# Kernel tuning notes

Hardware: AMD Instinct MI355X
Metric: run time of the kernel (lower is better)

The kernel has to match this reference:

```python
import jax, jax.numpy as jnp
import numpy as np

N_NODES = 100000
N_EDGES = 1600000
IN_CH = 128
HID = 128
OUT_CH = 64
N_GRAPHS = 512


def gcn_conv(x, edge_index, W, b):
    # GCNConv (PyG defaults): add self-loops, symmetric normalization
    # out = D^{-1/2} (A + I) D^{-1/2} X W + b
    n = x.shape[0]
    loop = jnp.arange(n, dtype=edge_index.dtype)
    src = jnp.concatenate([edge_index[0], loop])
    dst = jnp.concatenate([edge_index[1], loop])
    deg = jax.ops.segment_sum(jnp.ones_like(dst, x.dtype), dst, num_segments=n)
    dinv = jnp.where(deg > 0, jax.lax.rsqrt(deg), jnp.zeros_like(deg))
    norm = dinv[src] * dinv[dst]            # [E+N]
    h = x @ W                                # [N, out] transform first (dense GEMM)
    msg = h[src] * norm[:, None]             # gather + scale  [E+N, out]
    return jax.ops.segment_sum(msg, dst, num_segments=n) + b


def global_mean_pool(x, batch, num_graphs):
    sums = jax.ops.segment_sum(x, batch, num_segments=num_graphs)
    cnts = jax.ops.segment_sum(jnp.ones_like(batch, x.dtype), batch, num_segments=num_graphs)
    return sums / jnp.maximum(cnts, 1.0)[:, None]


def setup_inputs() -> dict:
    key = jax.random.key(0)
    ks = jax.random.split(key, 12)
    x = jax.random.normal(ks[0], (N_NODES, IN_CH), dtype=jnp.float32)
    edge_index = jax.random.randint(ks[1], (2, N_EDGES), 0, N_NODES, dtype=jnp.int64)
    batch = jnp.sort(jax.random.randint(ks[2], (N_NODES,), 0, N_GRAPHS, dtype=jnp.int64))
    def glorot(k, fi, fo):
        s = float(np.sqrt(6.0 / (fi + fo)))
        return jax.random.uniform(k, (fi, fo), jnp.float32, -s, s)
    W1 = glorot(ks[3], IN_CH, HID); b1 = jnp.zeros((HID,), jnp.float32)
    W2 = glorot(ks[4], HID, HID);   b2 = jnp.zeros((HID,), jnp.float32)
    W3 = glorot(ks[5], HID, HID);   b3 = jnp.zeros((HID,), jnp.float32)
    W4 = glorot(ks[6], HID, OUT_CH); b4 = jnp.zeros((OUT_CH,), jnp.float32)
    return {"x": x, "edge_index": edge_index, "batch": batch,
            "W1": W1, "b1": b1, "W2": W2, "b2": b2,
            "W3": W3, "b3": b3, "W4": W4, "b4": b4}


def reference(x, edge_index, batch, W1, b1, W2, b2, W3, b3, W4, b4):
    h = jax.nn.relu(gcn_conv(x, edge_index, W1, b1))
    h = jax.nn.relu(gcn_conv(h, edge_index, W2, b2))
    g = global_mean_pool(h, batch, N_GRAPHS)           # [G, HID]
    # MLP head; Dropout(0.2) is identity in eval mode
    g = jax.nn.relu(g @ W3 + b3)
    return g @ W4 + b4                                  # [G, OUT_CH]
```

## Files before the change

kernel.cpp:

```cpp
#include <hip/hip_runtime.h>

#define NN 100000
#define EE 1600000
#define CH 128
#define NG 512
#define OC 64

#define CSH 10
#define NCB 98
#define PBLK 256
#define PCHUNK 6250
#define SCAP 128
#define NCG 8
#define CPG 32
#define DSL 100352

#define O_DINV   0
#define O_ROWS   100032
#define O_CNT    200064
#define O_PART   225152
#define O_OFFS   225280
#define O_START  225408
#define O_CSR    225984
#define O_HS     2726016
#define O_STG    9126080
#define O_A1     14800448
#define O_DEG8   21200448
#define O_DEG    22003264
#define O_WT1    22103616
#define O_WT2    22120000

typedef __attribute__((ext_vector_type(8))) short short8v;
typedef __attribute__((ext_vector_type(4))) float float4v;

static __device__ __forceinline__ unsigned short f2bf(float x) {
  unsigned u = __float_as_uint(x);
  return (unsigned short)((u + 0x7FFFu + ((u >> 16) & 1u)) >> 16);
}
static __device__ __forceinline__ float bf2f(unsigned short h) {
  return __uint_as_float((unsigned)h << 16);
}
static __device__ __forceinline__ unsigned pack2(float a, float b) {
  return (unsigned)f2bf(a) | ((unsigned)f2bf(b) << 16);
}
static __device__ __forceinline__ float bflo(unsigned v) {
  return __uint_as_float(v << 16);
}
static __device__ __forceinline__ float bfhi(unsigned v) {
  return __uint_as_float(v & 0xFFFF0000u);
}

__global__ __launch_bounds__(1024) void k_part(const int* __restrict__ src,
                                               const int* __restrict__ dst,
                                               int* __restrict__ cnt,
                                               unsigned* __restrict__ stg) {
  __shared__ int hist[NCB];
  __shared__ int lcur[NCB];
  __shared__ unsigned lout[PCHUNK];
  int t = threadIdx.x;
  int e0 = blockIdx.x * PCHUNK;
  if (t < NCB) { hist[t] = 0; lcur[t] = 0; }
  __syncthreads();
  for (int e = e0 + t; e < e0 + PCHUNK; e += 1024)
    atomicAdd(&hist[dst[e] >> CSH], 1);
  __syncthreads();
  if (t == 0) {
    int s = 0;
    for (int i = 0; i < NCB; ++i) { int v = hist[i]; hist[i] = s; s += v; }
  }
  __syncthreads();
  for (int e = e0 + t; e < e0 + PCHUNK; e += 1024) {
    int d = dst[e];
    int b = d >> CSH;
    int p = hist[b] + atomicAdd(&lcur[b], 1);
    lout[p] = (unsigned)src[e] | ((unsigned)(d & 1023) << 17);
  }
  __syncthreads();
  int w = t >> 6, lane = t & 63;
  unsigned* mystg = stg + (size_t)blockIdx.x * NCB * SCAP;
  for (int b = w; b < NCB; b += 16) {
    int beg = hist[b];
    int end = (b == NCB - 1) ? PCHUNK : hist[b + 1];
    int n = min(end - beg, SCAP);
    for (int i = lane; i < n; i += 64) mystg[b * SCAP + i] = lout[beg + i];
    if (lane == 0) cnt[blockIdx.x * NCB + b] = n;
  }
}

__global__ __launch_bounds__(1024) void k_count2(const unsigned* __restrict__ stg,
                                                 const int* __restrict__ cnt,
                                                 int* __restrict__ deg8) {
  __shared__ int ldeg[1024];
  int b = blockIdx.x, g = blockIdx.y;
  int t = threadIdx.x;
  int w = t >> 6, lane = t & 63;
  ldeg[t] = 0;
  __syncthreads();
  for (int blk = g * CPG + w; blk < (g + 1) * CPG; blk += 16) {
    int c = cnt[blk * NCB + b];
    const unsigned* p = stg + ((size_t)blk * NCB + b) * SCAP;
    for (int e = lane; e < c; e += 64) atomicAdd(&ldeg[p[e] >> 17], 1);
  }
  __syncthreads();
  deg8[g * DSL + (b << CSH) + t] = ldeg[t];
}

__global__ __launch_bounds__(1024) void k_scan1(const int* __restrict__ deg8,
                                                int* __restrict__ deg,
                                                int* __restrict__ rows,
                                                int* __restrict__ part,
                                                float* __restrict__ dinv) {
  __shared__ int s[1024];
  int b = blockIdx.x, t = threadIdx.x;
  int gid = (b << CSH) + t;
  int v = 0;
#pragma unroll
  for (int g = 0; g < NCG; ++g) v += deg8[g * DSL + gid];
  if (gid < NN) {
    dinv[gid] = rsqrtf((float)(v + 1));
    deg[gid] = v;
  }
  int pdeg = (v + 7) & ~7;
  s[t] = pdeg;
  __syncthreads();
  for (int off = 1; off < 1024; off <<= 1) {
    int u = (t >= off) ? s[t - off] : 0;
    __syncthreads();
    if (t >= off) s[t] += u;
    __syncthreads();
  }
  if (gid < NN) rows[gid] = s[t] - pdeg;
  if (t == 1023) part[b] = s[t];
}

__global__ void k_scan_part(const int* __restrict__ part, int* __restrict__ offs) {
  __shared__ int s[128];
  int t = threadIdx.x;
  int v = (t < NCB) ? part[t] : 0;
  s[t] = v;
  __syncthreads();
  for (int off = 1; off < 128; off <<= 1) {
    int u = (t >= off) ? s[t - off] : 0;
    __syncthreads();
    if (t >= off) s[t] += u;
    __syncthreads();
  }
  if (t < NCB) offs[t] = s[t] - v;
}

__global__ void k_scan_add(int* __restrict__ rows, const int* __restrict__ offs,
                           const int* __restrict__ part, const int* __restrict__ deg,
                           const int* __restrict__ batch, int* __restrict__ start,
                           int* __restrict__ csr,
                           const float* __restrict__ W1, const float* __restrict__ W2,
                           unsigned short* __restrict__ wt1,
                           unsigned short* __restrict__ wt2) {
  int i = blockIdx.x * 256 + threadIdx.x;
  if (i >= NN) return;
  if (i < 32768) {
    const float* W = (i < 16384) ? W1 : W2;
    unsigned short* wt = (i < 16384) ? wt1 : wt2;
    int ii = i & 16383;
    int k = ii >> 7, n = ii & 127;
    float w = W[ii];
    unsigned short h = f2bf(w);
    unsigned short l = f2bf(w - bf2f(h));
    wt[n * 128 + k] = h;
    wt[16384 + n * 128 + k] = l;
  }
  int r = rows[i] + offs[i >> 10];
  rows[i] = r;
  if (i == 0) rows[NN] = offs[NCB - 1] + part[NCB - 1];
  int d = deg[i];
  int pd = (d + 7) & ~7;
  for (int k = r + d; k < r + pd; ++k) csr[k] = NN;
  int b = batch[i];
  int prev = (i == 0) ? -1 : batch[i - 1];
  for (int g = prev + 1; g <= b; ++g) start[g] = i;
  if (i == NN - 1)
    for (int g = b + 1; g <= NG; ++g) start[g] = NN;
}

__global__ __launch_bounds__(1024) void k_place2(const unsigned* __restrict__ stg,
                                                 const int* __restrict__ cnt,
                                                 const int* __restrict__ rows,
                                                 const int* __restrict__ deg8,
                                                 int* __restrict__ csr) {
  __shared__ int lrow[1024];
  __shared__ int lcur[1024];
  int b = blockIdx.x, g = blockIdx.y;
  int t = threadIdx.x;
  int w = t >> 6, lane = t & 63;
  int gid = (b << CSH) + t;
  int base = (gid < NN) ? rows[gid] : 0;
  for (int gp = 0; gp < g; ++gp) base += deg8[gp * DSL + gid];
  lrow[t] = base;
  lcur[t] = 0;
  __syncthreads();
  for (int blk = g * CPG + w; blk < (g + 1) * CPG; blk += 16) {
    int c = cnt[blk * NCB + b];
    const unsigned* p = stg + ((size_t)blk * NCB + b) * SCAP;
    for (int e = lane; e < c; e += 64) {
      unsigned x = p[e];
      int ld = x >> 17;
      int q = atomicAdd(&lcur[ld], 1);
      csr[lrow[ld] + q] = (int)(x & 0x1FFFFu);
    }
  }
}

__global__ __launch_bounds__(256) void k_gemm_mfma(
    const float* __restrict__ X, const unsigned short* __restrict__ wth,
    const unsigned short* __restrict__ wtl, const float* __restrict__ dinv,
    unsigned short* __restrict__ Hs) {
  __shared__ __align__(16) unsigned short sWh[64 * 136];
  __shared__ __align__(16) unsigned short sWl[64 * 136];
  __shared__ __align__(16) unsigned short sXh[128 * 40];
  __shared__ __align__(16) unsigned short sXl[128 * 40];

  const int t = threadIdx.x;
  const int w = t >> 6, lane = t & 63;
  const int quad = lane >> 4, lr = lane & 15;
  const int row0 = blockIdx.x * 128;
  const int col0 = blockIdx.y * 64;

  if (blockIdx.x == 0 && blockIdx.y == 0 && t < 64)
    *(unsigned*)&Hs[(size_t)NN * CH + t * 2] = 0u;

#pragma unroll
  for (int j = 0; j < 8; ++j) {
    int id = t + j * 256;
    int n = id >> 5, kk = (id & 31) * 4;
    *(ushort4*)&sWh[n * 136 + kk] = *(const ushort4*)&wth[(col0 + n) * 128 + kk];
    *(ushort4*)&sWl[n * 136 + kk] = *(const ushort4*)&wtl[(col0 + n) * 128 + kk];
  }

  float4v acc[2][4];
#pragma unroll
  for (int mi = 0; mi < 2; ++mi)
#pragma unroll
    for (int ni = 0; ni < 4; ++ni) acc[mi][ni] = (float4v){0.f, 0.f, 0.f, 0.f};

  for (int ks = 0; ks < 4; ++ks) {
    const int k0 = ks * 32;
    if (ks) __syncthreads();
#pragma unroll
    for (int i = 0; i < 4; ++i) {
      int row = i * 32 + (t >> 3);
      int seg = t & 7;
      int gr = row0 + row;
      float4 xv = {0.f, 0.f, 0.f, 0.f};
      if (gr < NN) xv = *(const float4*)&X[(size_t)gr * CH + k0 + seg * 4];
      ushort4 h, l;
      h.x = f2bf(xv.x); l.x = f2bf(xv.x - bf2f(h.x));
      h.y = f2bf(xv.y); l.y = f2bf(xv.y - bf2f(h.y));
      h.z = f2bf(xv.z); l.z = f2bf(xv.z - bf2f(h.z));
      h.w = f2bf(xv.w); l.w = f2bf(xv.w - bf2f(h.w));
      *(ushort4*)&sXh[row * 40 + seg * 4] = h;
      *(ushort4*)&sXl[row * 40 + seg * 4] = l;
    }
    __syncthreads();

    short8v ah[2], al[2];
#pragma unroll
    for (int mi = 0; mi < 2; ++mi) {
      int r = w * 32 + mi * 16 + lr;
      ah[mi] = *(const short8v*)&sXh[r * 40 + quad * 8];
      al[mi] = *(const short8v*)&sXl[r * 40 + quad * 8];
    }
#pragma unroll
    for (int ni = 0; ni < 4; ++ni) {
      int n = ni * 16 + lr;
      short8v bh = *(const short8v*)&sWh[n * 136 + k0 + quad * 8];
      short8v bl = *(const short8v*)&sWl[n * 136 + k0 + quad * 8];
#pragma unroll
      for (int mi = 0; mi < 2; ++mi) {
        acc[mi][ni] = __builtin_amdgcn_mfma_f32_16x16x32_bf16(ah[mi], bh, acc[mi][ni], 0, 0, 0);
        acc[mi][ni] = __builtin_amdgcn_mfma_f32_16x16x32_bf16(ah[mi], bl, acc[mi][ni], 0, 0, 0);
        acc[mi][ni] = __builtin_amdgcn_mfma_f32_16x16x32_bf16(al[mi], bh, acc[mi][ni], 0, 0, 0);
      }
    }
  }

#pragma unroll
  for (int mi = 0; mi < 2; ++mi) {
#pragma unroll
    for (int r = 0; r < 4; ++r) {
      int grow = row0 + w * 32 + mi * 16 + quad * 4 + r;
      if (grow < NN) {
        float d = dinv[grow];
#pragma unroll
        for (int ni = 0; ni < 4; ++ni)
          Hs[(size_t)grow * CH + col0 + ni * 16 + lr] = f2bf(d * acc[mi][ni][r]);
      }
    }
  }
}

__global__ __launch_bounds__(256) void k_gemm_bf(
    const unsigned short* __restrict__ A, const unsigned short* __restrict__ wth,
    const unsigned short* __restrict__ wtl, const float* __restrict__ dinv,
    unsigned short* __restrict__ Hs) {
  __shared__ __align__(16) unsigned short sWh[128 * 136];
  __shared__ __align__(16) unsigned short sWl[128 * 136];
  __shared__ __align__(16) unsigned short sA[128 * 40];

  const int t = threadIdx.x;
  const int w = t >> 6, lane = t & 63;
  const int quad = lane >> 4, lr = lane & 15;
  const int row0 = blockIdx.x * 128;

  if (blockIdx.x == 0 && t < 64)
    *(unsigned*)&Hs[(size_t)NN * CH + t * 2] = 0u;

#pragma unroll
  for (int j = 0; j < 16; ++j) {
    int id = t + j * 256;
    int n = id >> 5, kk = (id & 31) * 4;
    *(ushort4*)&sWh[n * 136 + kk] = *(const ushort4*)&wth[n * 128 + kk];
    *(ushort4*)&sWl[n * 136 + kk] = *(const ushort4*)&wtl[n * 128 + kk];
  }

  float4v acc[2][8];
#pragma unroll
  for (int mi = 0; mi < 2; ++mi)
#pragma unroll
    for (int ni = 0; ni < 8; ++ni) acc[mi][ni] = (float4v){0.f, 0.f, 0.f, 0.f};

  for (int ks = 0; ks < 4; ++ks) {
    const int k0 = ks * 32;
    if (ks) __syncthreads();
#pragma unroll
    for (int i = 0; i < 2; ++i) {
      int id = t + i * 256;
      int row = id >> 2, seg = id & 3;
      int gr = row0 + row;
      ushort4 v = {0, 0, 0, 0};
      if (gr < NN) v = *(const ushort4*)&A[(size_t)gr * CH + k0 + seg * 8];
      *(ushort4*)&sA[row * 40 + seg * 8] = v;
      ushort4 v2 = {0, 0, 0, 0};
      if (gr < NN) v2 = *(const ushort4*)&A[(size_t)gr * CH + k0 + seg * 8 + 4];
      *(ushort4*)&sA[row * 40 + seg * 8 + 4] = v2;
    }
    __syncthreads();

    short8v ah[2];
#pragma unroll
    for (int mi = 0; mi < 2; ++mi) {
      int r = w * 32 + mi * 16 + lr;
      ah[mi] = *(const short8v*)&sA[r * 40 + quad * 8];
    }
#pragma unroll
    for (int ni = 0; ni < 8; ++ni) {
      int n = ni * 16 + lr;
      short8v bh = *(const short8v*)&sWh[n * 136 + k0 + quad * 8];
      short8v bl = *(const short8v*)&sWl[n * 136 + k0 + quad * 8];
#pragma unroll
      for (int mi = 0; mi < 2; ++mi) {
        acc[mi][ni] = __builtin_amdgcn_mfma_f32_16x16x32_bf16(ah[mi], bh, acc[mi][ni], 0, 0, 0);
        acc[mi][ni] = __builtin_amdgcn_mfma_f32_16x16x32_bf16(ah[mi], bl, acc[mi][ni], 0, 0, 0);
      }
    }
  }

#pragma unroll
  for (int mi = 0; mi < 2; ++mi) {
#pragma unroll
    for (int r = 0; r < 4; ++r) {
      int grow = row0 + w * 32 + mi * 16 + quad * 4 + r;
      if (grow < NN) {
        float d = dinv[grow];
#pragma unroll
        for (int ni = 0; ni < 8; ++ni)
          Hs[(size_t)grow * CH + ni * 16 + lr] = f2bf(d * acc[mi][ni][r]);
      }
    }
  }
}

__global__ __launch_bounds__(256) void k_aggregate(
    const uint2* __restrict__ H2, const int* __restrict__ rows,
    const int* __restrict__ csr, const float* __restrict__ dinv,
    const float* __restrict__ bias, uint2* __restrict__ out) {
  int node = blockIdx.x * 4 + (threadIdx.x >> 6);
  if (node >= NN) return;
  int lane = threadIdx.x & 63;
  int h = lane >> 5, li = lane & 31;
  float a0 = 0.f, a1 = 0.f, a2 = 0.f, a3 = 0.f;
  int e0 = rows[node], e1 = rows[node + 1];
  int nr = (e1 - e0) >> 3;
  if (nr) {
    const int* cp = csr + e0 + h;
    uint2 va[4], vb[4];

#define LOADQ(buf)                                                          \
  do {                                                                      \
    unsigned s0_ = (unsigned)cp[0], s1_ = (unsigned)cp[2];                  \
    unsigned s2_ = (unsigned)cp[4], s3_ = (unsigned)cp[6];                  \
    buf[0] = H2[(s0_ << 5) | li];                                           \
    buf[1] = H2[(s1_ << 5) | li];                                           \
    buf[2] = H2[(s2_ << 5) | li];                                           \
    buf[3] = H2[(s3_ << 5) | li];                                           \
    cp += 8;                                                                \
  } while (0)

#define ACCQ(buf)                                                           \
  do {                                                                      \
    _Pragma("unroll")                                                       \
    for (int k_ = 0; k_ < 4; ++k_) {                                        \
      a0 += bflo(buf[k_].x); a1 += bfhi(buf[k_].x);                         \
      a2 += bflo(buf[k_].y); a3 += bfhi(buf[k_].y);                         \
    }                                                                       \
  } while (0)

    LOADQ(va);
    int rem = nr - 1;
    while (rem >= 2) {
      LOADQ(vb); ACCQ(va);
      LOADQ(va); ACCQ(vb);
      rem -= 2;
    }
    if (rem) { LOADQ(vb); ACCQ(va); ACCQ(vb); }
    else     { ACCQ(va); }
#undef LOADQ
#undef ACCQ
  }
  a0 += __shfl_xor(a0, 32);
  a1 += __shfl_xor(a1, 32);
  a2 += __shfl_xor(a2, 32);
  a3 += __shfl_xor(a3, 32);
  uint2 sv = H2[((unsigned)node << 5) | li];
  a0 += bflo(sv.x); a1 += bfhi(sv.x);
  a2 += bflo(sv.y); a3 += bfhi(sv.y);
  float d = dinv[node];
  float4 b4 = *(const float4*)&bias[li << 2];
  float o0 = fmaxf(fmaf(d, a0, b4.x), 0.f);
  float o1 = fmaxf(fmaf(d, a1, b4.y), 0.f);
  float o2 = fmaxf(fmaf(d, a2, b4.z), 0.f);
  float o3 = fmaxf(fmaf(d, a3, b4.w), 0.f);
  if (!h)
    out[((unsigned)node << 5) | li] = make_uint2(pack2(o0, o1), pack2(o2, o3));
}

__global__ __launch_bounds__(256) void k_head(
    const unsigned short* __restrict__ A, const int* __restrict__ start,
    const float* __restrict__ W3, const float* __restrict__ b3,
    const float* __restrict__ W4, const float* __restrict__ b4,
    float* __restrict__ out) {
  __shared__ float ppart[16][128];
  __shared__ float pooled[128];
  __shared__ float g1[128];
  int g = blockIdx.x;
  int t = threadIdx.x;
  int c8 = t & 15;
  int r = t >> 4;
  int s0 = start[g], s1 = start[g + 1];
  float s[8] = {0.f, 0.f, 0.f, 0.f, 0.f, 0.f, 0.f, 0.f};
  for (int i = s0 + r; i < s1; i += 16) {
    short8v v = *(const short8v*)&A[(size_t)i * CH + c8 * 8];
#pragma unroll
    for (int j = 0; j < 8; ++j) s[j] += bf2f((unsigned short)v[j]);
  }
#pragma unroll
  for (int j = 0; j < 8; ++j) ppart[r][c8 * 8 + j] = s[j];
  __syncthreads();
  if (t < 128) {
    float n = fmaxf((float)(s1 - s0), 1.0f);
    float acc = 0.f;
#pragma unroll
    for (int rr = 0; rr < 16; ++rr) acc += ppart[rr][t];
    pooled[t] = acc / n;
  }
  __syncthreads();
  if (t < 128) {
    float acc = b3[t];
    for (int k = 0; k < 128; ++k) acc += pooled[k] * W3[k * CH + t];
    g1[t] = fmaxf(acc, 0.f);
  }
  __syncthreads();
  if (t < 64) {
    float acc = b4[t];
    for (int k = 0; k < 128; ++k) acc += g1[k] * W4[k * OC + t];
    out[(size_t)g * OC + t] = acc;
  }
}

extern "C" void kernel_launch(void* const* d_in, const int* in_sizes, int n_in,
                              void* d_out, int out_size, void* d_ws, size_t ws_size,
                              hipStream_t stream) {
  const float* X   = (const float*)d_in[0];
  const int* ei    = (const int*)d_in[1];
  const int* batch = (const int*)d_in[2];
  const float* W1  = (const float*)d_in[3];
  const float* b1  = (const float*)d_in[4];
  const float* W2  = (const float*)d_in[5];
  const float* b2  = (const float*)d_in[6];
  const float* W3  = (const float*)d_in[7];
  const float* b3  = (const float*)d_in[8];
  const float* W4  = (const float*)d_in[9];
  const float* b4  = (const float*)d_in[10];
  float* out = (float*)d_out;
  float* ws = (float*)d_ws;

  const int* src = ei;
  const int* dst = ei + EE;

  float* dinv = ws + O_DINV;
  int* rows   = (int*)(ws + O_ROWS);
  int* cnt    = (int*)(ws + O_CNT);
  int* part   = (int*)(ws + O_PART);
  int* offs   = (int*)(ws + O_OFFS);
  int* start  = (int*)(ws + O_START);
  int* csr    = (int*)(ws + O_CSR);
  unsigned short* Hs = (unsigned short*)(ws + O_HS);
  unsigned* stg = (unsigned*)(ws + O_STG);
  unsigned short* wt1 = (unsigned short*)(ws + O_WT1);
  unsigned short* wt2 = (unsigned short*)(ws + O_WT2);
  unsigned short* A1 = (unsigned short*)(ws + O_A1);
  int* deg8   = (int*)(ws + O_DEG8);
  int* deg    = (int*)(ws + O_DEG);

  k_part<<<PBLK, 1024, 0, stream>>>(src, dst, cnt, stg);
  k_count2<<<dim3(NCB, NCG), 1024, 0, stream>>>(stg, cnt, deg8);
  k_scan1<<<NCB, 1024, 0, stream>>>(deg8, deg, rows, part, dinv);
  k_scan_part<<<1, 128, 0, stream>>>(part, offs);
  k_scan_add<<<(NN + 255) / 256, 256, 0, stream>>>(rows, offs, part, deg, batch,
                                                   start, csr, W1, W2, wt1, wt2);
  k_place2<<<dim3(NCB, NCG), 1024, 0, stream>>>(stg, cnt, rows, deg8, csr);

  dim3 ggrid((NN + 127) / 128, 2);
  k_gemm_mfma<<<ggrid, 256, 0, stream>>>(X, wt1, wt1 + 16384, dinv, Hs);
  k_aggregate<<<(NN + 3) / 4, 256, 0, stream>>>((const uint2*)Hs, rows, csr, dinv, b1, (uint2*)A1);
  k_gemm_bf<<<(NN + 127) / 128, 256, 0, stream>>>(A1, wt2, wt2 + 16384, dinv, Hs);
  k_aggregate<<<(NN + 3) / 4, 256, 0, stream>>>((const uint2*)Hs, rows, csr, dinv, b2, (uint2*)A1);

  k_head<<<NG, 256, 0, stream>>>(A1, start, W3, b3, W4, b4, out);
}
```

Baseline: 344.9 us.

## Fuse partition-offset scan into scan_add and widen first GEMM to full 128 columns

Removes the single-block k_scan_part launch. Each k_scan_add block now computes its own bucket offset by reducing the preceding partition totals (four blocks share one 1024-node bucket). Separately, the first-layer GEMM now uses 512-thread blocks that cover all 128 output columns, instead of two 64-column blocks per row tile. This means the fp32 X rows are loaded and split into bf16 hi/lo once rather than twice. The cost is a redundant small reduction in every scan block and a larger LDS footprint per GEMM block, which may lower occupancy.

```diff
diff --git a/kernel.cpp b/kernel.cpp
--- a/kernel.cpp
+++ b/kernel.cpp
@@ -19,7 +19,6 @@
 #define O_ROWS   100032
 #define O_CNT    200064
 #define O_PART   225152
-#define O_OFFS   225280
 #define O_START  225408
 #define O_CSR    225984
 #define O_HS     2726016
@@ -133,28 +132,23 @@
   if (t == 1023) part[b] = s[t];
 }
 
-__global__ void k_scan_part(const int* __restrict__ part, int* __restrict__ offs) {
-  __shared__ int s[128];
-  int t = threadIdx.x;
-  int v = (t < NCB) ? part[t] : 0;
-  s[t] = v;
-  __syncthreads();
-  for (int off = 1; off < 128; off <<= 1) {
-    int u = (t >= off) ? s[t - off] : 0;
+__global__ __launch_bounds__(256) void k_scan_add(
+    int* __restrict__ rows, const int* __restrict__ part,
+    const int* __restrict__ deg, const int* __restrict__ batch,
+    int* __restrict__ start, int* __restrict__ csr,
+    const float* __restrict__ W1, const float* __restrict__ W2,
+    unsigned short* __restrict__ wt1, unsigned short* __restrict__ wt2) {
+  __shared__ int red[256];
+  int bkt = blockIdx.x >> 2;
+  int partial = 0;
+  for (int j = threadIdx.x; j < bkt; j += 256) partial += part[j];
+  red[threadIdx.x] = partial;
+  __syncthreads();
+  for (int off = 128; off; off >>= 1) {
+    if (threadIdx.x < off) red[threadIdx.x] += red[threadIdx.x + off];
     __syncthreads();
-    if (t >= off) s[t] += u;
-    __syncthreads();
-  }
-  if (t < NCB) offs[t] = s[t] - v;
-}
-
-__global__ void k_scan_add(int* __restrict__ rows, const int* __restrict__ offs,
-                           const int* __restrict__ part, const int* __restrict__ deg,
-                           const int* __restrict__ batch, int* __restrict__ start,
-                           int* __restrict__ csr,
-                           const float* __restrict__ W1, const float* __restrict__ W2,
-                           unsigned short* __restrict__ wt1,
-                           unsigned short* __restrict__ wt2) {
+  }
+  int boff = red[0];
   int i = blockIdx.x * 256 + threadIdx.x;
   if (i >= NN) return;
   if (i < 32768) {
@@ -168,9 +162,10 @@
     wt[n * 128 + k] = h;
     wt[16384 + n * 128 + k] = l;
   }
-  int r = rows[i] + offs[i >> 10];
+  int r = rows[i] + boff;
   rows[i] = r;
-  if (i == 0) rows[NN] = offs[NCB - 1] + part[NCB - 1];
+  if (blockIdx.x == 390 && threadIdx.x == 0)
+    rows[NN] = boff + part[NCB - 1];
   int d = deg[i];
   int pd = (d + 7) & ~7;
   for (int k = r + d; k < r + pd; ++k) csr[k] = NN;
@@ -209,30 +204,30 @@
   }
 }
 
-__global__ __launch_bounds__(256) void k_gemm_mfma(
+__global__ __launch_bounds__(512) void k_gemm_mfma(
     const float* __restrict__ X, const unsigned short* __restrict__ wth,
     const unsigned short* __restrict__ wtl, const float* __restrict__ dinv,
     unsigned short* __restrict__ Hs) {
-  __shared__ __align__(16) unsigned short sWh[64 * 136];
-  __shared__ __align__(16) unsigned short sWl[64 * 136];
+  __shared__ __align__(16) unsigned short sWh[128 * 136];
+  __shared__ __align__(16) unsigned short sWl[128 * 136];
   __shared__ __align__(16) unsigned short sXh[128 * 40];
   __shared__ __align__(16) unsigned short sXl[128 * 40];
 
   const int t = threadIdx.x;
   const int w = t >> 6, lane = t & 63;
   const int quad = lane >> 4, lr = lane & 15;
+  const int wr = w & 3, wc = w >> 2;
   const int row0 = blockIdx.x * 128;
-  const int col0 = blockIdx.y * 64;
-
-  if (blockIdx.x == 0 && blockIdx.y == 0 && t < 64)
+
+  if (blockIdx.x == 0 && t < 64)
     *(unsigned*)&Hs[(size_t)NN * CH + t * 2] = 0u;
 
 #pragma unroll
   for (int j = 0; j < 8; ++j) {
-    int id = t + j * 256;
+    int id = t + j * 512;
     int n = id >> 5, kk = (id & 31) * 4;
-    *(ushort4*)&sWh[n * 136 + kk] = *(const ushort4*)&wth[(col0 + n) * 128 + kk];
-    *(ushort4*)&sWl[n * 136 + kk] = *(const ushort4*)&wtl[(col0 + n) * 128 + kk];
+    *(ushort4*)&sWh[n * 136 + kk] = *(const ushort4*)&wth[n * 128 + kk];
+    *(ushort4*)&sWl[n * 136 + kk] = *(const ushort4*)&wtl[n * 128 + kk];
   }
 
   float4v acc[2][4];
@@ -245,8 +240,8 @@
     const int k0 = ks * 32;
     if (ks) __syncthreads();
 #pragma unroll
-    for (int i = 0; i < 4; ++i) {
-      int row = i * 32 + (t >> 3);
+    for (int i = 0; i < 2; ++i) {
+      int row = i * 64 + (t >> 3);
       int seg = t & 7;
       int gr = row0 + row;
       float4 xv = {0.f, 0.f, 0.f, 0.f};
@@ -264,13 +259,13 @@
     short8v ah[2], al[2];
 #pragma unroll
     for (int mi = 0; mi < 2; ++mi) {
-      int r = w * 32 + mi * 16 + lr;
+      int r = wr * 32 + mi * 16 + lr;
       ah[mi] = *(const short8v*)&sXh[r * 40 + quad * 8];
       al[mi] = *(const short8v*)&sXl[r * 40 + quad * 8];
     }
 #pragma unroll
     for (int ni = 0; ni < 4; ++ni) {
-      int n = ni * 16 + lr;
+      int n = wc * 64 + ni * 16 + lr;
       short8v bh = *(const short8v*)&sWh[n * 136 + k0 + quad * 8];
       short8v bl = *(const short8v*)&sWl[n * 136 + k0 + quad * 8];
 #pragma unroll
@@ -286,12 +281,12 @@
   for (int mi = 0; mi < 2; ++mi) {
 #pragma unroll
     for (int r = 0; r < 4; ++r) {
-      int grow = row0 + w * 32 + mi * 16 + quad * 4 + r;
+      int grow = row0 + wr * 32 + mi * 16 + quad * 4 + r;
       if (grow < NN) {
         float d = dinv[grow];
 #pragma unroll
         for (int ni = 0; ni < 4; ++ni)
-          Hs[(size_t)grow * CH + col0 + ni * 16 + lr] = f2bf(d * acc[mi][ni][r]);
+          Hs[(size_t)grow * CH + wc * 64 + ni * 16 + lr] = f2bf(d * acc[mi][ni][r]);
       }
     }
   }
@@ -509,7 +504,6 @@
   int* rows   = (int*)(ws + O_ROWS);
   int* cnt    = (int*)(ws + O_CNT);
   int* part   = (int*)(ws + O_PART);
-  int* offs   = (int*)(ws + O_OFFS);
   int* start  = (int*)(ws + O_START);
   int* csr    = (int*)(ws + O_CSR);
   unsigned short* Hs = (unsigned short*)(ws + O_HS);
@@ -523,13 +517,11 @@
   k_part<<<PBLK, 1024, 0, stream>>>(src, dst, cnt, stg);
   k_count2<<<dim3(NCB, NCG), 1024, 0, stream>>>(stg, cnt, deg8);
   k_scan1<<<NCB, 1024, 0, stream>>>(deg8, deg, rows, part, dinv);
-  k_scan_part<<<1, 128, 0, stream>>>(part, offs);
-  k_scan_add<<<(NN + 255) / 256, 256, 0, stream>>>(rows, offs, part, deg, batch,
+  k_scan_add<<<(NN + 255) / 256, 256, 0, stream>>>(rows, part, deg, batch,
                                                    start, csr, W1, W2, wt1, wt2);
   k_place2<<<dim3(NCB, NCG), 1024, 0, stream>>>(stg, cnt, rows, deg8, csr);
 
-  dim3 ggrid((NN + 127) / 128, 2);
-  k_gemm_mfma<<<ggrid, 256, 0, stream>>>(X, wt1, wt1 + 16384, dinv, Hs);
+  k_gemm_mfma<<<(NN + 127) / 128, 512, 0, stream>>>(X, wt1, wt1 + 16384, dinv, Hs);
   k_aggregate<<<(NN + 3) / 4, 256, 0, stream>>>((const uint2*)Hs, rows, csr, dinv, b1, (uint2*)A1);
   k_gemm_bf<<<(NN + 127) / 128, 256, 0, stream>>>(A1, wt2, wt2 + 16384, dinv, Hs);
   k_aggregate<<<(NN + 3) / 4, 256, 0, stream>>>((const uint2*)Hs, rows, csr, dinv, b2, (uint2*)A1);
```

New measurement: 334.0 us. -3.2%, faster.
